# Kernel tuning notes

Measured on AMD Instinct MI355X. Metric: run time of the kernel, lower is better.

Reference implementation:

```python
import jax, jax.numpy as jnp
import numpy as np

_SAMPLING_EPS = 1e-5
B, V = 256, 128000


def _apply_min_p(logits, min_p):
    # probs >= min_p * max_prob  <=>  keep; else logit -> -inf
    probs = jax.nn.softmax(logits, axis=-1)
    max_probs = jnp.max(probs, axis=-1, keepdims=True)
    keep = probs >= (min_p[:, None] * max_probs)
    return jnp.where(keep, logits, -jnp.inf)


def _apply_top_k_top_p(logits, top_k, top_p):
    # Sort ascending once; derive per-row keep-thresholds for both filters.
    logits_sort = jnp.sort(logits, axis=-1)  # [B, V] ascending
    # top-k threshold: value at position V-k (kth largest)
    k_idx = jnp.clip(V - top_k, 0, V - 1).astype(jnp.int32)
    k_thresh = jnp.take_along_axis(logits_sort, k_idx[:, None], axis=-1)  # [B,1]
    # top-p: on ascending-sorted probs, token is kept iff cumsum > 1 - p
    probs_sort = jax.nn.softmax(logits_sort, axis=-1)
    probs_cum = jnp.cumsum(probs_sort, axis=-1)
    kept = probs_cum > (1.0 - top_p[:, None])
    kept = kept.at[:, -1].set(True)  # always keep the max-prob token
    p_thresh = jnp.min(jnp.where(kept, logits_sort, jnp.inf), axis=-1, keepdims=True)
    thresh = jnp.maximum(k_thresh, p_thresh)
    return jnp.where(logits >= thresh, logits, -jnp.inf)


def setup_inputs() -> dict:
    key = jax.random.key(0)
    k1, k2, k3, k4, k5 = jax.random.split(key, 5)
    logits = jax.random.normal(k1, (B, V), jnp.float32)
    temperature = jax.random.uniform(k2, (B,), jnp.float32, 0.1, 1.5)
    temperature = temperature.at[:8].set(0.0)  # greedy rows
    min_p = jax.random.uniform(k3, (B,), jnp.float32, 0.0, 0.2)
    top_k = jax.random.randint(k4, (B,), 1, 64).astype(jnp.int32)
    top_p = jax.random.uniform(k5, (B,), jnp.float32, 0.5, 1.0)
    return {"logits": logits, "temperature": temperature, "min_p": min_p,
            "top_k": top_k, "top_p": top_p}


def reference(logits, temperature, min_p, top_k, top_p):
    logits = logits.astype(jnp.float32)
    greedy = jnp.argmax(logits, axis=-1)  # [B]
    # safe temperature divide (greedy rows have temp ~ 0 but are overridden)
    safe_t = jnp.where(temperature < _SAMPLING_EPS, 1.0, temperature)
    scaled = logits / safe_t[:, None]
    scaled = _apply_min_p(scaled, min_p)
    masked = _apply_top_k_top_p(scaled, top_k, top_p)
    # Gumbel-max trick == categorical sampling from softmax(masked)
    u = jax.random.uniform(jax.random.key(42), masked.shape, jnp.float32, 1e-10, 1.0)
    gumbel = -jnp.log(-jnp.log(u))
    random_sampled = jnp.argmax(masked + gumbel, axis=-1)
    sampled = jnp.where(temperature < _SAMPLING_EPS, greedy, random_sampled)
    return sampled[:, None]  # sampled_token_ids [B, 1]
```

## Files before the change

### kernel.cpp

```cpp
#include <hip/hip_runtime.h>
#include <stdint.h>

typedef unsigned long long u64;
typedef unsigned int u32;

#define VOCAB 128000
#define NV4   32000
#define NROWS 256
#define BLK   1024
#define NW    16
#define NB    4096
#define CAPL  2048
#define SEPS  1e-5f
#define LN2X40 27.725887222397812f

__device__ __forceinline__ u32 f2key(float f){
  u32 u = __float_as_uint(f);
  return (u & 0x80000000u) ? ~u : (u | 0x80000000u);
}
__device__ __forceinline__ float key2f(u32 k){
  u32 u = (k & 0x80000000u) ? (k ^ 0x80000000u) : ~k;
  return __uint_as_float(u);
}

__device__ __forceinline__ void tf2x32(u32 x0, u32 x1, u32 &o0, u32 &o1){
  const u32 k0 = 0u, k1 = 42u, k2 = 0u ^ 42u ^ 0x1BD11BDAu;
  x0 += k0; x1 += k1;
#define TFR(r) { x0 += x1; x1 = (x1 << (r)) | (x1 >> (32 - (r))); x1 ^= x0; }
  TFR(13) TFR(15) TFR(26) TFR(6)
  x0 += k1; x1 += k2 + 1u;
  TFR(17) TFR(29) TFR(16) TFR(24)
  x0 += k2; x1 += k0 + 2u;
  TFR(13) TFR(15) TFR(26) TFR(6)
  x0 += k0; x1 += k1 + 3u;
  TFR(17) TFR(29) TFR(16) TFR(24)
  x0 += k1; x1 += k2 + 4u;
  TFR(13) TFR(15) TFR(26) TFR(6)
  x0 += k2; x1 += k0 + 5u;
#undef TFR
  o0 = x0; o1 = x1;
}
__device__ __forceinline__ u32 gumbel_bits(u32 i){
  u32 o0, o1; tf2x32(0u, i, o0, o1);
  return o0 ^ o1;
}
__device__ __forceinline__ float bits2gumbel(u32 b){
  float f = __uint_as_float(0x3F800000u | (b >> 9)) - 1.0f;
  float u = fmaxf(1e-10f, f + 1e-10f);
  return -logf(-logf(u));
}

__device__ __forceinline__ void cross4096_u32(
    const u32* arr, u32* aux, u32 target, u32* out_idx, u32* out_before, int t)
{
  aux[t] = arr[4*t+0] + arr[4*t+1] + arr[4*t+2] + arr[4*t+3];
  __syncthreads();
  if (t < 64){
    u32 gs = 0u;
    #pragma unroll
    for (int j=0;j<16;j++) gs += aux[t*16+j];
    u32 pref = gs;
    #pragma unroll
    for (int d=1; d<64; d<<=1){ u32 v = __shfl_up(pref, d, 64); if (t >= d) pref += v; }
    u64 bal = __ballot(pref > target);
    int g = bal ? (__ffsll((long long)bal) - 1) : 63;
    u32 pg = __shfl(pref, g, 64);
    u32 gg = __shfl(gs, g, 64);
    if (t == 0){
      u32 c = pg - gg;
      u32 idx = (u32)(g*64 + 63);
      for (int j=0;j<16;j++){
        u32 v = aux[g*16+j];
        if (c + v > target){
          int base = (g*16+j)*4;
          for (int q=0;q<4;q++){
            u32 w = arr[base+q];
            if (c + w > target){ idx = (u32)(base+q); goto doneu; }
            c += w;
          }
        }
        c += v;
      }
      doneu:
      *out_idx = idx; *out_before = c;
    }
  }
}

__device__ __forceinline__ void cross4096_u64(
    const u64* arr, u64* aux, u64 target, u32* out_idx, u64* out_before, int t)
{
  aux[t] = arr[4*t+0] + arr[4*t+1] + arr[4*t+2] + arr[4*t+3];
  __syncthreads();
  if (t < 64){
    u64 gs = 0ull;
    #pragma unroll
    for (int j=0;j<16;j++) gs += aux[t*16+j];
    u64 pref = gs;
    #pragma unroll
    for (int d=1; d<64; d<<=1){
      u64 v = __shfl_up((unsigned long long)pref, d, 64); if (t >= d) pref += v;
    }
    u64 bal = __ballot(pref > target);
    int g = bal ? (__ffsll((long long)bal) - 1) : 63;
    u64 pg = __shfl((unsigned long long)pref, g, 64);
    u64 gg = __shfl((unsigned long long)gs, g, 64);
    if (t == 0){
      u64 c = pg - gg;
      u32 idx = (u32)(g*64 + 63);
      for (int j=0;j<16;j++){
        u64 v = aux[g*16+j];
        if (c + v > target){
          int base = (g*16+j)*4;
          for (int q=0;q<4;q++){
            u64 w = arr[base+q];
            if (c + w > target){ idx = (u32)(base+q); goto donev; }
            c += w;
          }
        }
        c += v;
      }
      donev:
      *out_idx = idx; *out_before = c;
    }
  }
}

__device__ __forceinline__ void cross4096_mass(
    const u64* arr, u64* aux, float topp_v, u64* out_target,
    u32* out_idx, u64* out_before, int t)
{
  aux[t] = arr[4*t+0] + arr[4*t+1] + arr[4*t+2] + arr[4*t+3];
  __syncthreads();
  if (t < 64){
    u64 gs = 0ull;
    #pragma unroll
    for (int j=0;j<16;j++) gs += aux[t*16+j];
    u64 pref = gs;
    #pragma unroll
    for (int d=1; d<64; d<<=1){
      u64 v = __shfl_up((unsigned long long)pref, d, 64); if (t >= d) pref += v;
    }
    u64 total = __shfl((unsigned long long)pref, 63, 64);
    u64 target = (u64)((double)(1.0f - topp_v) * (double)total);
    u64 bal = __ballot(pref > target);
    int g = bal ? (__ffsll((long long)bal) - 1) : 63;
    u64 pg = __shfl((unsigned long long)pref, g, 64);
    u64 gg = __shfl((unsigned long long)gs, g, 64);
    if (t == 0){
      u64 c = pg - gg;
      u32 idx = (u32)(g*64 + 63);
      for (int j=0;j<16;j++){
        u64 v = aux[g*16+j];
        if (c + v > target){
          int base = (g*16+j)*4;
          for (int q=0;q<4;q++){
            u64 w = arr[base+q];
            if (c + w > target){ idx = (u32)(base+q); goto donem; }
            c += w;
          }
        }
        c += v;
      }
      donem:
      *out_target = target; *out_idx = idx; *out_before = c;
    }
  }
}

__device__ __forceinline__ void cross256_u32(const u32* arr, u32 target, u32* out_idx, int t){
  if (t < 64){
    u32 gs = arr[4*t+0]+arr[4*t+1]+arr[4*t+2]+arr[4*t+3];
    u32 pref = gs;
    #pragma unroll
    for (int d=1; d<64; d<<=1){ u32 v=__shfl_up(pref,d,64); if (t>=d) pref+=v; }
    u64 bal = __ballot(pref > target);
    int g = bal ? (__ffsll((long long)bal)-1) : 63;
    u32 pg=__shfl(pref,g,64), gg=__shfl(gs,g,64);
    if (t==0){
      u32 c = pg-gg; u32 idx=(u32)(g*4+3);
      for (int q=0;q<4;q++){ u32 w=arr[g*4+q]; if (c+w>target){ idx=(u32)(g*4+q); break; } c+=w; }
      *out_idx = idx;
    }
  }
}
__device__ __forceinline__ void cross256_u64(const u64* arr, u64 target, u32* out_idx, int t){
  if (t < 64){
    u64 gs = arr[4*t+0]+arr[4*t+1]+arr[4*t+2]+arr[4*t+3];
    u64 pref = gs;
    #pragma unroll
    for (int d=1; d<64; d<<=1){
      u64 v=__shfl_up((unsigned long long)pref,d,64); if (t>=d) pref+=v;
    }
    u64 bal = __ballot(pref > target);
    int g = bal ? (__ffsll((long long)bal)-1) : 63;
    u64 pg=__shfl((unsigned long long)pref,g,64), gg=__shfl((unsigned long long)gs,g,64);
    if (t==0){
      u64 c = pg-gg; u32 idx=(u32)(g*4+3);
      for (int q=0;q<4;q++){ u64 w=arr[g*4+q]; if (c+w>target){ idx=(u32)(g*4+q); break; } c+=w; }
      *out_idx = idx;
    }
  }
}

__device__ __forceinline__ void argmax_write(
    float best, u32 bi, float* wrf, u32* wru, int ln, int wv, int b, int* out)
{
  #pragma unroll
  for (int d=32; d>0; d>>=1){
    float c2=__shfl_down(best,d,64); u32 i2=__shfl_down(bi,d,64);
    if (c2>best || (c2==best && i2<bi)){best=c2;bi=i2;}
  }
  if (ln==0){ wrf[wv]=best; wru[wv]=bi; }
  __syncthreads();
  if (wv==0){
    float b1=(ln<NW)?wrf[ln]:-INFINITY; u32 i1=(ln<NW)?wru[ln]:0xFFFFFFFFu;
    #pragma unroll
    for (int d=32; d>0; d>>=1){
      float b2=__shfl_down(b1,d,64); u32 i2=__shfl_down(i1,d,64);
      if (b2>b1 || (b2==b1 && i2<i1)){b1=b2;i1=i2;}
    }
    if (ln==0) out[b]=(int)i1;
  }
}

__global__ __launch_bounds__(BLK) void k_all(
    const float* __restrict__ logits, const float* __restrict__ temp,
    const float* __restrict__ minp, const int* __restrict__ topk,
    const float* __restrict__ topp, int* __restrict__ out)
{
  __shared__ u32 cnt[NB];
  __shared__ u64 massI[NB];
  __shared__ u64 list[CAPL];
  __shared__ u64 aux64[BLK];
  __shared__ float wrf1[NW];
  __shared__ u32  wru1[NW], wru2[NW];
  __shared__ u32 sh_kmax, sh_lstar, sh_len, sh_idx, sh_bef32, sh_u1, sh_u2, sh_u3;
  __shared__ float sh_Z;
  __shared__ u64 sh_bef64, sh_tfix;

  u32* aux32 = (u32*)aux64;

  const int b = blockIdx.x;
  const int t = threadIdx.x;
  const int ln = t & 63, wv = t >> 6;
  const float T = temp[b];
  const float* row = logits + (size_t)b * VOCAB;
  const float4* row4 = (const float4*)row;

  if (T < SEPS){
    float M = -INFINITY; u32 Mi = 0xFFFFFFFFu;
    for (int i=t; i<NV4; i+=BLK){
      float4 q = row4[i];
      #pragma unroll
      for (int j=0;j<4;j++){
        float l = (&q.x)[j]; u32 gi = (u32)(i*4+j);
        if (l > M){ M = l; Mi = gi; }
      }
    }
    argmax_write(M, Mi, wrf1, wru1, ln, wv, b, out);
    return;
  }

  const float invT = 1.0f / T;
  for (int i=t;i<NB;i+=BLK){ cnt[i]=0u; massI[i]=0ull; }
  if (t==0) sh_len=0u;
  __syncthreads();

  u32 km = 0u;
  float S0=0.0f,S1=0.0f,S2=0.0f,S3=0.0f;
#define P1E(LV, SS) { \
    float l_ = (LV); u32 k_ = f2key(l_); \
    if (k_ > km) km = k_; \
    atomicAdd(&cnt[k_>>20], 1u); \
    SS += __expf(l_ * invT); }
  for (int i=t; i<NV4; i+=2*BLK){
    float4 qa = row4[i];
    int i2 = i + BLK; bool h2 = (i2 < NV4);
    float4 qb; if (h2) qb = row4[i2];
    P1E(qa.x,S0) P1E(qa.y,S1) P1E(qa.z,S2) P1E(qa.w,S3)
    if (h2){ P1E(qb.x,S0) P1E(qb.y,S1) P1E(qb.z,S2) P1E(qb.w,S3) }
  }
#undef P1E
  float S = (S0+S1)+(S2+S3);
  #pragma unroll
  for (int d=32; d>0; d>>=1){
    S += __shfl_down(S, d, 64);
    u32 k2 = __shfl_down(km, d, 64); if (k2 > km) km = k2;
  }
  if (ln==0){ wrf1[wv]=S; wru1[wv]=km; }
  __syncthreads();
  if (t==0){
    float St=0.0f; u32 kt=0u;
    for (int w=0; w<NW; w++){ St += wrf1[w]; if (wru1[w]>kt) kt=wru1[w]; }
    sh_kmax = kt;
    sh_Z = St;
  }
  __syncthreads();
  const float m = key2f(sh_kmax) * invT;
  const float Z = sh_Z * __expf(-m);

  int tk = topk[b]; if (tk < 1) tk = 1; if (tk > VOCAB) tk = VOCAB;
  cross4096_u32(cnt, aux32, (u32)(VOCAB - tk), &sh_idx, &sh_bef32, t);
  __syncthreads();
  const u32 b1k = sh_idx;
  const u32 r1  = (u32)(VOCAB - tk + 1) - sh_bef32;

  if (wv==0){
    const float rhs = minp[b] * (1.0f / Z);
    u32 lo = 0u, hi = 0xFF800000u;
    while (hi - lo > 64u){
      u32 step = (hi - lo) >> 6;
      u32 k = lo + (u32)(ln + 1) * step;
      float e = __expf(fmaf(key2f(k), invT, -m));
      u64 bal = __ballot((e / Z) >= rhs);
      if (bal){
        u32 g = (u32)(__ffsll((long long)bal) - 1);
        hi = lo + (g + 1u) * step;
        lo = lo + g * step;
      } else {
        lo += 64u * step;
      }
    }
    u32 k = lo + 1u + (u32)ln;
    bool ok = (k <= hi);
    float e = __expf(fmaf(key2f(k), invT, -m));
    u64 bal = __ballot(ok && ((e / Z) >= rhs));
    if (ln==0) sh_lstar = bal ? (lo + 1u + (u32)(__ffsll((long long)bal) - 1)) : hi;
  }
  __syncthreads();
  const u32 lstar = sh_lstar;
  const u32 bl = lstar >> 20;

  {
    u32 pa=0u, pc=0u;
    for (int i=t;i<NB;i+=BLK){
      u32 c = cnt[i];
      if ((u32)i > bl)   pa += c;
      if ((u32)i >= b1k) pc += c;
    }
    #pragma unroll
    for (int d=32; d>0; d>>=1){ pa += __shfl_down(pa,d,64); pc += __shfl_down(pc,d,64); }
    if (ln==0){ wru1[wv]=pa; wru2[wv]=pc; }
    __syncthreads();
    if (t==0){
      u32 a=0u, c2=0u;
      for (int w=0; w<NW; w++){ a += wru1[w]; c2 += wru2[w]; }
      sh_u1 = a; sh_u2 = c2;
    }
    __syncthreads();
  }
  const u32 Kmin = sh_u1;
  const bool kcert = (Kmin >= (u32)tk);
  const u32 CLB = kcert ? b1k : bl;
  const u32 listlen = kcert ? sh_u2 : (Kmin + cnt[bl]);
  const bool fastOK = (listlen <= (u32)CAPL);
  const float cs = LN2X40 - m;

  u32 kc = 0u;
#define P2E(LV, IDX) { \
    float l_ = (LV); u32 key_ = f2key(l_); \
    if (key_ >= lstar){ \
      kc++; \
      u64 lm_ = (u64)__expf(fmaf(l_, invT, cs)); \
      if (lm_) atomicAdd(&massI[key_>>20], lm_); \
    } \
    if (fastOK && (key_>>20) >= CLB){ \
      u32 p_ = atomicAdd(&sh_len, 1u); \
      if (p_ < CAPL) list[p_] = ((u64)key_ << 32) | (u64)(u32)(IDX); \
    } \
  }
  for (int i=t; i<NV4; i+=2*BLK){
    float4 qa = row4[i];
    int i2 = i + BLK; bool h2 = (i2 < NV4);
    float4 qb; if (h2) qb = row4[i2];
    P2E(qa.x, i*4+0) P2E(qa.y, i*4+1) P2E(qa.z, i*4+2) P2E(qa.w, i*4+3)
    if (h2){
      P2E(qb.x, i2*4+0) P2E(qb.y, i2*4+1) P2E(qb.z, i2*4+2) P2E(qb.w, i2*4+3)
    }
  }
#undef P2E
  #pragma unroll
  for (int d=32; d>0; d>>=1) kc += __shfl_down(kc, d, 64);
  if (ln==0) wru1[wv] = kc;
  __syncthreads();
  if (t==0){ u32 K2=0u; for (int w=0;w<NW;w++) K2 += wru1[w]; sh_u3 = K2; }
  __syncthreads();
  const u32 K = sh_u3;
  const bool kval = (K >= (u32)tk);
  const u32 llen = (sh_len <= (u32)CAPL) ? sh_len : (u32)CAPL;

  cross4096_mass(massI, aux64, topp[b], &sh_tfix, &sh_idx, &sh_bef64, t);
  __syncthreads();
  const u32 b1p = sh_idx;
  const u64 t1  = sh_tfix - sh_bef64;
  const bool needK = kval && (b1p <= b1k);
  const bool needP = (!kval) || (b1p >= b1k);

  u32 kkey = 0u, pkey = 0u;

  if (fastOK){
    if (needK){
      for (int i=t;i<NB;i+=BLK) cnt[i]=0u;
      __syncthreads();
      for (u32 i=t; i<llen; i+=BLK){
        u32 key = (u32)(list[i]>>32);
        if ((key>>20) == b1k) atomicAdd(&cnt[(key>>8)&0xFFFu], 1u);
      }
      __syncthreads();
      cross4096_u32(cnt, aux32, r1-1u, &sh_idx, &sh_bef32, t);
      __syncthreads();
      u32 b2k = sh_idx, r2 = r1 - sh_bef32;
      u32 prefk = (b1k<<12) | b2k;
      for (int i=t;i<256;i+=BLK) cnt[i]=0u;
      __syncthreads();
      for (u32 i=t; i<llen; i+=BLK){
        u32 key = (u32)(list[i]>>32);
        if ((key>>8) == prefk) atomicAdd(&cnt[key&0xFFu], 1u);
      }
      __syncthreads();
      cross256_u32(cnt, r2-1u, &sh_idx, t);
      __syncthreads();
      kkey = (prefk<<8) | sh_idx;
    }
    if (needP){
      for (int i=t;i<NB;i+=BLK) massI[i]=0ull;
      __syncthreads();
      for (u32 i=t; i<llen; i+=BLK){
        u32 key = (u32)(list[i]>>32);
        if ((key>>20) == b1p && key >= lstar){
          u64 lm = (u64)__expf(fmaf(key2f(key), invT, cs));
          if (lm) atomicAdd(&massI[(key>>8)&0xFFFu], lm);
        }
      }
      __syncthreads();
      cross4096_u64(massI, aux64, t1, &sh_idx, &sh_bef64, t);
      __syncthreads();
      u32 b2p = sh_idx; u64 t2 = t1 - sh_bef64;
      u32 prefp = (b1p<<12) | b2p;
      for (int i=t;i<256;i+=BLK) massI[i]=0ull;
      __syncthreads();
      for (u32 i=t; i<llen; i+=BLK){
        u32 key = (u32)(list[i]>>32);
        if ((key>>8) == prefp && key >= lstar){
          u64 lm = (u64)__expf(fmaf(key2f(key), invT, cs));
          if (lm) atomicAdd(&massI[key&0xFFu], lm);
        }
      }
      __syncthreads();
      cross256_u64(massI, t2, &sh_idx, t);
      __syncthreads();
      pkey = (prefp<<8) | sh_idx;
    }
    const u32 thrkey = kkey > pkey ? kkey : pkey;

    float best = -INFINITY; u32 bi = 0xFFFFFFFFu;
    for (u32 i=t; i<llen; i+=BLK){
      u64 e = list[i];
      u32 key = (u32)(e>>32);
      if (key >= thrkey){
        u32 idx = (u32)e;
        u32 c = (u32)b * (u32)VOCAB + idx;
        float cand = key2f(key)*invT + bits2gumbel(gumbel_bits(c));
        if (cand > best || (cand == best && idx < bi)){ best = cand; bi = idx; }
      }
    }
    argmax_write(best, bi, wrf1, wru1, ln, wv, b, out);
    return;
  }

  for (int i=t;i<NB;i+=BLK){ cnt[i]=0u; massI[i]=0ull; }
  __syncthreads();
  for (int i=t; i<NV4; i+=BLK){
    float4 q = row4[i];
    #pragma unroll
    for (int j=0;j<4;j++){
      float l = (&q.x)[j]; u32 key = f2key(l); u32 hb = key>>20;
      if (needK && hb == b1k) atomicAdd(&cnt[(key>>8)&0xFFFu], 1u);
      if (needP && hb == b1p && key >= lstar){
        u64 lm = (u64)__expf(fmaf(l, invT, cs));
        if (lm) atomicAdd(&massI[(key>>8)&0xFFFu], lm);
      }
    }
  }
  __syncthreads();
  u32 b2k = 0u, r2 = 1u, b2p = 0u; u64 t2 = 0ull;
  if (needK){
    cross4096_u32(cnt, aux32, r1-1u, &sh_idx, &sh_bef32, t);
    __syncthreads();
    b2k = sh_idx; r2 = r1 - sh_bef32;
  }
  if (needP){
    cross4096_u64(massI, aux64, t1, &sh_idx, &sh_bef64, t);
    __syncthreads();
    b2p = sh_idx; t2 = t1 - sh_bef64;
  }
  const u32 prefk = (b1k<<12) | b2k;
  const u32 prefp = (b1p<<12) | b2p;
  for (int i=t;i<256;i+=BLK){ cnt[i]=0u; massI[i]=0ull; }
  __syncthreads();
  for (int i=t; i<NV4; i+=BLK){
    float4 q = row4[i];
    #pragma unroll
    for (int j=0;j<4;j++){
      float l = (&q.x)[j]; u32 key = f2key(l);
      if (needK && (key>>8) == prefk) atomicAdd(&cnt[key&0xFFu], 1u);
      if (needP && (key>>8) == prefp && key >= lstar){
        u64 lm = (u64)__expf(fmaf(l, invT, cs));
        if (lm) atomicAdd(&massI[key&0xFFu], lm);
      }
    }
  }
  __syncthreads();
  if (needK){
    cross256_u32(cnt, r2-1u, &sh_idx, t);
    __syncthreads();
    kkey = (prefk<<8) | sh_idx;
  }
  if (needP){
    cross256_u64(massI, t2, &sh_idx, t);
    __syncthreads();
    pkey = (prefp<<8) | sh_idx;
  }
  const float thrf = key2f(kkey > pkey ? kkey : pkey);
  float best = -INFINITY; u32 bi = 0xFFFFFFFFu;
  for (int i=t; i<NV4; i+=BLK){
    float4 q = row4[i];
    #pragma unroll
    for (int j=0;j<4;j++){
      float l = (&q.x)[j];
      if (l >= thrf){
        u32 idx = (u32)(i*4+j);
        u32 c = (u32)b * (u32)VOCAB + idx;
        float cand = l*invT + bits2gumbel(gumbel_bits(c));
        if (cand > best || (cand == best && idx < bi)){ best = cand; bi = idx; }
      }
    }
  }
  argmax_write(best, bi, wrf1, wru1, ln, wv, b, out);
}

extern "C" void kernel_launch(void* const* d_in, const int* in_sizes, int n_in,
                              void* d_out, int out_size, void* d_ws, size_t ws_size,
                              hipStream_t stream)
{
  const float* logits = (const float*)d_in[0];
  const float* temp   = (const float*)d_in[1];
  const float* minp   = (const float*)d_in[2];
  const int*   topk   = (const int*)d_in[3];
  const float* topp   = (const float*)d_in[4];
  int* out = (int*)d_out;

  hipLaunchKernelGGL(k_all, dim3(NROWS), dim3(BLK), 0, stream,
                     logits, temp, minp, topk, topp, out);
}
```

Baseline: 57.36 us.

## Sample a speculative threshold to build candidate list during first pass

Adds a pre-pass that histograms 2048 sampled logits per row to pick a speculative high-value bucket threshold. The first pass then only counts histogram entries and appends list entries for candidates above that threshold, using wave-aggregated atomics instead of per-element atomics. The second pass no longer builds the list or needs the extra count reduction. If too few candidates are captured, it falls back to a full histogram rescan, and CAPL grows to 8192, which increases LDS use and may lower occupancy.

```diff
diff --git a/kernel.cpp b/kernel.cpp
--- a/kernel.cpp
+++ b/kernel.cpp
@@ -10,7 +10,7 @@
 #define BLK   1024
 #define NW    16
 #define NB    4096
-#define CAPL  2048
+#define CAPL  8192
 #define SEPS  1e-5f
 #define LN2X40 27.725887222397812f
 
@@ -235,7 +235,7 @@
   __shared__ u64 aux64[BLK];
   __shared__ float wrf1[NW];
   __shared__ u32  wru1[NW], wru2[NW];
-  __shared__ u32 sh_kmax, sh_lstar, sh_len, sh_idx, sh_bef32, sh_u1, sh_u2, sh_u3;
+  __shared__ u32 sh_kmax, sh_lstar, sh_len, sh_idx, sh_bef32;
   __shared__ float sh_Z;
   __shared__ u64 sh_bef64, sh_tfix;
 
@@ -261,25 +261,49 @@
     argmax_write(M, Mi, wrf1, wru1, ln, wv, b, out);
     return;
   }
-
   const float invT = 1.0f / T;
+
+  for (int i=t;i<NB;i+=BLK) cnt[i]=0u;
+  if (t==0) sh_len=0u;
+  __syncthreads();
+  for (int s=t; s<2048; s+=BLK){
+    int c = s >> 6, j = s & 63;
+    atomicAdd(&cnt[f2key(row[c*4000 + j])>>20], 1u);
+  }
+  __syncthreads();
+  cross4096_u32(cnt, aux32, 2016u, &sh_idx, &sh_bef32, t);
+  __syncthreads();
+  const u32 bspec = sh_idx;
+  const u32 keyspec = bspec << 20;
+  __syncthreads();
   for (int i=t;i<NB;i+=BLK){ cnt[i]=0u; massI[i]=0ull; }
-  if (t==0) sh_len=0u;
   __syncthreads();
 
   u32 km = 0u;
   float S0=0.0f,S1=0.0f,S2=0.0f,S3=0.0f;
-#define P1E(LV, SS) { \
+#define P1E(LV, SS, IDX) { \
     float l_ = (LV); u32 k_ = f2key(l_); \
     if (k_ > km) km = k_; \
-    atomicAdd(&cnt[k_>>20], 1u); \
-    SS += __expf(l_ * invT); }
+    SS += __expf(l_ * invT); \
+    bool cand_ = (k_ >= keyspec); \
+    u64 bal_ = __ballot(cand_); \
+    if (cand_){ \
+      atomicAdd(&cnt[k_>>20], 1u); \
+      u32 lead_ = (u32)__ffsll((long long)bal_) - 1u; \
+      u32 base_ = 0u; \
+      if ((u32)ln == lead_) base_ = atomicAdd(&sh_len, (u32)__popcll(bal_)); \
+      base_ = __shfl(base_, (int)lead_, 64); \
+      u32 p_ = base_ + (u32)__popcll(bal_ & ((1ull << ln) - 1ull)); \
+      if (p_ < CAPL) list[p_] = ((u64)k_ << 32) | (u64)(u32)(IDX); \
+    } }
   for (int i=t; i<NV4; i+=2*BLK){
     float4 qa = row4[i];
     int i2 = i + BLK; bool h2 = (i2 < NV4);
     float4 qb; if (h2) qb = row4[i2];
-    P1E(qa.x,S0) P1E(qa.y,S1) P1E(qa.z,S2) P1E(qa.w,S3)
-    if (h2){ P1E(qb.x,S0) P1E(qb.y,S1) P1E(qb.z,S2) P1E(qb.w,S3) }
+    P1E(qa.x,S0,i*4+0) P1E(qa.y,S1,i*4+1) P1E(qa.z,S2,i*4+2) P1E(qa.w,S3,i*4+3)
+    if (h2){
+      P1E(qb.x,S0,i2*4+0) P1E(qb.y,S1,i2*4+1) P1E(qb.z,S2,i2*4+2) P1E(qb.w,S3,i2*4+3)
+    }
   }
 #undef P1E
   float S = (S0+S1)+(S2+S3);
@@ -299,12 +323,28 @@
   __syncthreads();
   const float m = key2f(sh_kmax) * invT;
   const float Z = sh_Z * __expf(-m);
+  const u32 Nc = sh_len;
 
   int tk = topk[b]; if (tk < 1) tk = 1; if (tk > VOCAB) tk = VOCAB;
-  cross4096_u32(cnt, aux32, (u32)(VOCAB - tk), &sh_idx, &sh_bef32, t);
+  const bool sampleOK = (Nc >= (u32)tk);
+  u32 NcEff = Nc;
+  if (!sampleOK){
+    __syncthreads();
+    for (int i=t;i<NB;i+=BLK) cnt[i]=0u;
+    __syncthreads();
+    for (int i=t; i<NV4; i+=BLK){
+      float4 q = row4[i];
+      #pragma unroll
+      for (int j=0;j<4;j++) atomicAdd(&cnt[f2key((&q.x)[j])>>20], 1u);
+    }
+    __syncthreads();
+    NcEff = (u32)VOCAB;
+  }
+
+  cross4096_u32(cnt, aux32, NcEff - (u32)tk, &sh_idx, &sh_bef32, t);
   __syncthreads();
   const u32 b1k = sh_idx;
-  const u32 r1  = (u32)(VOCAB - tk + 1) - sh_bef32;
+  const u32 r1  = (NcEff - (u32)tk + 1u) - sh_bef32;
 
   if (wv==0){
     const float rhs = minp[b] * (1.0f / Z);
@@ -330,65 +370,33 @@
   }
   __syncthreads();
   const u32 lstar = sh_lstar;
-  const u32 bl = lstar >> 20;
-
-  {
-    u32 pa=0u, pc=0u;
-    for (int i=t;i<NB;i+=BLK){
-      u32 c = cnt[i];
-      if ((u32)i > bl)   pa += c;
-      if ((u32)i >= b1k) pc += c;
-    }
-    #pragma unroll
-    for (int d=32; d>0; d>>=1){ pa += __shfl_down(pa,d,64); pc += __shfl_down(pc,d,64); }
-    if (ln==0){ wru1[wv]=pa; wru2[wv]=pc; }
-    __syncthreads();
-    if (t==0){
-      u32 a=0u, c2=0u;
-      for (int w=0; w<NW; w++){ a += wru1[w]; c2 += wru2[w]; }
-      sh_u1 = a; sh_u2 = c2;
-    }
-    __syncthreads();
-  }
-  const u32 Kmin = sh_u1;
-  const bool kcert = (Kmin >= (u32)tk);
-  const u32 CLB = kcert ? b1k : bl;
-  const u32 listlen = kcert ? sh_u2 : (Kmin + cnt[bl]);
-  const bool fastOK = (listlen <= (u32)CAPL);
+  const bool fastOK = sampleOK && (Nc <= (u32)CAPL);
   const float cs = LN2X40 - m;
 
   u32 kc = 0u;
-#define P2E(LV, IDX) { \
+#define P2E(LV) { \
     float l_ = (LV); u32 key_ = f2key(l_); \
     if (key_ >= lstar){ \
       kc++; \
       u64 lm_ = (u64)__expf(fmaf(l_, invT, cs)); \
       if (lm_) atomicAdd(&massI[key_>>20], lm_); \
-    } \
-    if (fastOK && (key_>>20) >= CLB){ \
-      u32 p_ = atomicAdd(&sh_len, 1u); \
-      if (p_ < CAPL) list[p_] = ((u64)key_ << 32) | (u64)(u32)(IDX); \
-    } \
-  }
+    } }
   for (int i=t; i<NV4; i+=2*BLK){
     float4 qa = row4[i];
     int i2 = i + BLK; bool h2 = (i2 < NV4);
     float4 qb; if (h2) qb = row4[i2];
-    P2E(qa.x, i*4+0) P2E(qa.y, i*4+1) P2E(qa.z, i*4+2) P2E(qa.w, i*4+3)
-    if (h2){
-      P2E(qb.x, i2*4+0) P2E(qb.y, i2*4+1) P2E(qb.z, i2*4+2) P2E(qb.w, i2*4+3)
-    }
+    P2E(qa.x) P2E(qa.y) P2E(qa.z) P2E(qa.w)
+    if (h2){ P2E(qb.x) P2E(qb.y) P2E(qb.z) P2E(qb.w) }
   }
 #undef P2E
   #pragma unroll
   for (int d=32; d>0; d>>=1) kc += __shfl_down(kc, d, 64);
-  if (ln==0) wru1[wv] = kc;
-  __syncthreads();
-  if (t==0){ u32 K2=0u; for (int w=0;w<NW;w++) K2 += wru1[w]; sh_u3 = K2; }
-  __syncthreads();
-  const u32 K = sh_u3;
+  if (ln==0) wru2[wv] = kc;
+  __syncthreads();
+  if (t==0){ u32 K2=0u; for (int w=0;w<NW;w++) K2 += wru2[w]; wru2[0] = K2; }
+  __syncthreads();
+  const u32 K = wru2[0];
   const bool kval = (K >= (u32)tk);
-  const u32 llen = (sh_len <= (u32)CAPL) ? sh_len : (u32)CAPL;
 
   cross4096_mass(massI, aux64, topp[b], &sh_tfix, &sh_idx, &sh_bef64, t);
   __syncthreads();
@@ -400,6 +408,7 @@
   u32 kkey = 0u, pkey = 0u;
 
   if (fastOK){
+    const u32 llen = Nc;
     if (needK){
       for (int i=t;i<NB;i+=BLK) cnt[i]=0u;
       __syncthreads();
```

Result: slower. 73.32 us (+27.8%).
